# Kernel tuning notes

Measured on AMD Instinct MI355X. Metric: run time of the kernel, lower is better.

Reference implementation:

```python
import jax, jax.numpy as jnp
import numpy as np

B, S, D_MODEL, H = 2, 2048, 512, 8
DH = D_MODEL // H  # dim per head
NEG_INF = 1e9


def setup_inputs() -> dict:
    key = jax.random.key(0)
    ks = jax.random.split(key, 8)
    sc = 0.05
    return {
        "query": jax.random.normal(ks[0], (B, S, D_MODEL), jnp.float32),
        "key": jax.random.normal(ks[1], (B, S, D_MODEL), jnp.float32),
        "value": jax.random.normal(ks[2], (B, S, D_MODEL), jnp.float32),
        "mask": jnp.zeros((B, 1, S, S), jnp.float32),
        "wq": jax.random.normal(ks[3], (D_MODEL, D_MODEL), jnp.float32) * sc,
        "bq": jnp.zeros((D_MODEL,), jnp.float32),
        "wk": jax.random.normal(ks[4], (D_MODEL, D_MODEL), jnp.float32) * sc,
        "bk": jnp.zeros((D_MODEL,), jnp.float32),
        "wv": jax.random.normal(ks[5], (D_MODEL, D_MODEL), jnp.float32) * sc,
        "bv": jnp.zeros((D_MODEL,), jnp.float32),
        "wo": jax.random.normal(ks[6], (D_MODEL, D_MODEL), jnp.float32) * sc,
        "bo": jnp.zeros((D_MODEL,), jnp.float32),
    }


def _split_heads(x):
    # (B, S, D_MODEL) -> (B, H, S, DH)
    b, s, _ = x.shape
    return x.reshape(b, s, H, DH).transpose(0, 2, 1, 3)


def reference(query, key, value, mask, wq, bq, wk, bk, wv, bv, wo, bo):
    q = _split_heads(query @ wq + bq)
    k = _split_heads(key @ wk + bk)
    v = _split_heads(value @ wv + bv)
    # scaled dot-product attention; full (B, H, S, S) scores as in original
    scores = jnp.einsum("bhqd,bhkd->bhqk", q, k) / jnp.sqrt(jnp.float32(DH))
    scores = scores + mask * (-NEG_INF)
    weights = jax.nn.softmax(scores, axis=-1)  # dropout inactive (rate=0 / eval)
    attn = jnp.einsum("bhqk,bhkd->bhqd", weights, v)
    # merge heads: (B, H, S, DH) -> (B, S, D_MODEL)
    b = attn.shape[0]
    merged = attn.transpose(0, 2, 1, 3).reshape(b, -1, D_MODEL)
    return merged @ wo + bo
```

## Files before the change

### kernel.cpp

```cpp
#include <hip/hip_runtime.h>
#include <hip/hip_bf16.h>

typedef unsigned short u16;
typedef unsigned int u32;
typedef __bf16 bf16x8 __attribute__((ext_vector_type(8)));
typedef float f32x4 __attribute__((ext_vector_type(4)));
typedef u16 u16x8 __attribute__((ext_vector_type(8)));
typedef u32 u32x2 __attribute__((ext_vector_type(2)));

#define S_LEN 2048
#define DMODEL 512
#define NHEAD 8
#define DHEAD 64
#define QSCALE 0.1803368801111204f
#define MASKC 1.4426950409e9f
#define RESCALE_THR 8.0f

static __device__ __forceinline__ u16 f2bf(float f) {
    union { float f; unsigned u; } cv; cv.f = f;
    unsigned u = cv.u;
    return (u16)((u + 0x7fffu + ((u >> 16) & 1u)) >> 16);
}
static __device__ __forceinline__ u32 pk2bf(float a, float b) {
    union { __hip_bfloat162 h; u32 u; } cv;
    float2 f2; f2.x = a; f2.y = b;
    cv.h = __float22bfloat162_rn(f2);
    return cv.u;
}
static __device__ __forceinline__ bf16x8 ld8(const u16* p) {
    return *(const bf16x8*)p;
}
static __device__ __forceinline__ float fmax3(float a, float b, float c) {
    return __builtin_fmaxf(__builtin_fmaxf(a, b), c);
}

__global__ __launch_bounds__(256) void prep_kernel(
    const float* __restrict__ q, const float* __restrict__ k, const float* __restrict__ v,
    const float* __restrict__ w0, const float* __restrict__ w1,
    const float* __restrict__ w2, const float* __restrict__ w3,
    const float* __restrict__ mask,
    u16* __restrict__ Aqkv, u16* __restrict__ wtall, int* __restrict__ flags) {
    const int p = blockIdx.x;
    const int tid = threadIdx.x;
    __shared__ float t[32][33];
    __shared__ int wred[4];
    if (p < 3072) {
        const int z = p >> 10, px = p & 1023;
        const float* in = (z == 0) ? q : (z == 1) ? k : v;
        u16* o = Aqkv + (long)z * 2097152;
        long i = ((long)px * 256 + tid) * 8;
        f32x4 a = *(const f32x4*)(in + i);
        f32x4 b = *(const f32x4*)(in + i + 4);
        u16x8 r;
#pragma unroll
        for (int j = 0; j < 4; ++j) { r[j] = f2bf(a[j]); r[4 + j] = f2bf(b[j]); }
        *(u16x8*)(o + i) = r;
    } else if (p < 4096) {
        const int p2 = p - 3072;
        const int z = p2 >> 8, rem = p2 & 255, by = rem >> 4, bx = rem & 15;
        const float* in = (z == 0) ? w0 : (z == 1) ? w1 : (z == 2) ? w2 : w3;
        u16* o = wtall + (long)(((z + 1) & 3)) * 262144;
        const int tx = tid & 31, ty = tid >> 5;
#pragma unroll
        for (int i = 0; i < 4; ++i)
            t[ty + 8 * i][tx] = in[(by * 32 + ty + 8 * i) * DMODEL + bx * 32 + tx];
        __syncthreads();
#pragma unroll
        for (int i = 0; i < 4; ++i)
            o[(bx * 32 + ty + 8 * i) * DMODEL + by * 32 + tx] = f2bf(t[tx][ty + 8 * i]);
    } else {
        const int bid = p - 4096;
        const int b = bid >> 10, qt = (bid >> 5) & 31, kt = bid & 31;
        const int r = tid >> 2, cs = tid & 3;
        const float* mp = mask + ((long)(b * S_LEN + qt * 64 + r)) * S_LEN + kt * 64 + cs * 16;
        int nz = 0;
#pragma unroll
        for (int j = 0; j < 4; ++j) {
            f32x4 a = *(const f32x4*)(mp + j * 4);
            nz |= (a[0] != 0.f) | (a[1] != 0.f) | (a[2] != 0.f) | (a[3] != 0.f);
        }
        unsigned long long ball = __ballot(nz);
        if ((tid & 63) == 0) wred[tid >> 6] = (ball != 0ull) ? 1 : 0;
        __syncthreads();
        if (tid == 0) flags[bid] = wred[0] | wred[1] | wred[2] | wred[3];
    }
}

template <bool F32OUT, int TM>
static __device__ __forceinline__ void store_c(f32x4 (&acc)[TM][2],
                                               const float* __restrict__ bias,
                                               void* __restrict__ Cp, float oscale,
                                               bool vtout, int m0, int n0, int cidx, int kg) {
    if (vtout) {
        const int bb = m0 >> 11;
#pragma unroll
        for (int j = 0; j < 2; ++j) {
            int col = n0 + j * 16 + cidx;
            float bv = bias[col];
            u16* vt = (u16*)Cp + (((long)(bb * 8 + (col >> 6))) * 64 + (col & 63)) * S_LEN;
#pragma unroll
            for (int i = 0; i < TM; ++i) {
                int s = (m0 + i * 16 + kg * 4) & (S_LEN - 1);
                u32x2 d;
                d[0] = pk2bf(acc[i][j][0] + bv, acc[i][j][1] + bv);
                d[1] = pk2bf(acc[i][j][2] + bv, acc[i][j][3] + bv);
                *(u32x2*)(vt + s) = d;
            }
        }
        return;
    }
#pragma unroll
    for (int j = 0; j < 2; ++j) {
        int col = n0 + j * 16 + cidx;
        float bv = bias[col];
#pragma unroll
        for (int i = 0; i < TM; ++i) {
#pragma unroll
            for (int r = 0; r < 4; ++r) {
                int row = m0 + i * 16 + kg * 4 + r;
                float val = (acc[i][j][r] + bv) * oscale;
                if (F32OUT) {
                    ((float*)Cp)[(long)row * DMODEL + col] = val;
                } else {
                    ((u16*)Cp)[(long)row * DMODEL + col] = f2bf(val);
                }
            }
        }
    }
}

template <int BM, bool F32OUT>
static __device__ __forceinline__ void gemm_lds(const u16* __restrict__ Ag,
                                                const u16* __restrict__ Wg,
                                                const float* __restrict__ bias,
                                                void* __restrict__ Cp, float oscale,
                                                bool vtout, int bx, int by) {
    constexpr int MR = BM / 32;
    constexpr int NCH = BM / 64 + 1;
    __shared__ __align__(16) u16 As[2][BM][40];
    __shared__ __align__(16) u16 Bs[2][64][40];

    const int tid = threadIdx.x;
    const int lane = tid & 63;
    const int wave = tid >> 6;
    const int wr = wave >> 1, wc = wave & 1;
    const int cidx = lane & 15;
    const int kg = lane >> 4;

    const u16* gsrc[NCH];
    u16* ld0[NCH];
    u16* ld1[NCH];
#pragma unroll
    for (int j = 0; j < NCH; ++j) {
        int c = tid + 256 * j;
        if (c < BM * 4) {
            int r = c >> 2, s = c & 3;
            gsrc[j] = Ag + (long)(by * BM + r) * DMODEL + s * 8;
            ld0[j] = &As[0][r][s * 8];
            ld1[j] = &As[1][r][s * 8];
        } else {
            int c2 = c - BM * 4;
            int r = c2 >> 2, s = c2 & 3;
            gsrc[j] = Wg + (long)(bx * 64 + r) * DMODEL + s * 8;
            ld0[j] = &Bs[0][r][s * 8];
            ld1[j] = &Bs[1][r][s * 8];
        }
    }

    u16x8 rg[NCH];
#pragma unroll
    for (int j = 0; j < NCH; ++j) rg[j] = *(const u16x8*)(gsrc[j]);
#pragma unroll
    for (int j = 0; j < NCH; ++j) *(u16x8*)(ld0[j]) = rg[j];
#pragma unroll
    for (int j = 0; j < NCH; ++j) rg[j] = *(const u16x8*)(gsrc[j] + 32);
    __syncthreads();

    const f32x4 fz = {0.f, 0.f, 0.f, 0.f};
    f32x4 acc[MR][2];
#pragma unroll
    for (int i = 0; i < MR; ++i)
#pragma unroll
        for (int j = 0; j < 2; ++j) acc[i][j] = fz;

    const int mw = wr * (BM / 2);
    const int nw = wc * 32;

#pragma unroll 2
    for (int t = 0; t < 16; ++t) {
        const int cur = t & 1;
        if (t + 1 < 16) {
#pragma unroll
            for (int j = 0; j < NCH; ++j) *(u16x8*)((cur ? ld0 : ld1)[j]) = rg[j];
            if (t + 2 < 16) {
#pragma unroll
                for (int j = 0; j < NCH; ++j) rg[j] = *(const u16x8*)(gsrc[j] + (t + 2) * 32);
            }
        }
        bf16x8 a[MR], b[2];
#pragma unroll
        for (int i = 0; i < MR; ++i) a[i] = ld8(&As[cur][mw + i * 16 + cidx][kg * 8]);
#pragma unroll
        for (int j = 0; j < 2; ++j) b[j] = ld8(&Bs[cur][nw + j * 16 + cidx][kg * 8]);
        __builtin_amdgcn_s_setprio(1);
#pragma unroll
        for (int i = 0; i < MR; ++i)
#pragma unroll
            for (int j = 0; j < 2; ++j)
                acc[i][j] = __builtin_amdgcn_mfma_f32_16x16x32_bf16(a[i], b[j], acc[i][j], 0, 0, 0);
        __builtin_amdgcn_s_setprio(0);
        __syncthreads();
    }

    store_c<F32OUT, MR>(acc, bias, Cp, oscale, vtout, by * BM + mw, bx * 64 + nw, cidx, kg);
}

static __device__ __forceinline__ void xcd_swizzle(int gridX, int gridY, int& bx, int& by) {
    const int flat = blockIdx.x + gridX * blockIdx.y;
    const int xcd = flat & 7;
    const int j = flat >> 3;
    by = xcd * (gridY >> 3) + j / gridX;
    bx = j % gridX;
}

__global__ __launch_bounds__(256) void qkv_gemm_kernel(
    const u16* __restrict__ Aqkv,
    const u16* __restrict__ wtall,
    const float* __restrict__ bq, const float* __restrict__ bk, const float* __restrict__ bv,
    u16* __restrict__ Q, u16* __restrict__ K, u16* __restrict__ Vt) {
    const u16* A = Aqkv + (long)blockIdx.z * 2097152;
    const u16* W = wtall + (long)(blockIdx.z + 1) * 262144;
    const float* b;
    u16* C;
    float sc = 1.f;
    bool vt = false;
    if (blockIdx.z == 0) { b = bq; C = Q; sc = QSCALE; }
    else if (blockIdx.z == 1) { b = bk; C = K; }
    else { b = bv; C = Vt; vt = true; }
    int bx, by;
    xcd_swizzle(8, 32, bx, by);
    gemm_lds<128, false>(A, W, b, C, sc, vt, bx, by);
}

__global__ __launch_bounds__(256) void out_gemm_kernel(const u16* __restrict__ A,
                                                       const u16* __restrict__ Wt,
                                                       const float* __restrict__ bias,
                                                       float* __restrict__ C) {
    int bx, by;
    xcd_swizzle(8, 64, bx, by);
    gemm_lds<64, true>(A, Wt, bias, C, 1.f, false, bx, by);
}

__global__ __launch_bounds__(256) void attn_kernel(const u16* __restrict__ Q,
                                                   const u16* __restrict__ K,
                                                   const u16* __restrict__ Vt,
                                                   const float* __restrict__ mask,
                                                   const int* __restrict__ flags,
                                                   u16* __restrict__ Ab) {
    const int tid = threadIdx.x;
    const int lane = tid & 63;
    const int wave = tid >> 6;
    const int cidx = lane & 15;
    const int kg = lane >> 4;
    const int flat = blockIdx.x + 32 * blockIdx.y;
    const int F = (flat & 7) * 64 + (flat >> 3);
    const int qt = F & 31;
    const int bh = F >> 5;
    const int b = bh >> 3, h = bh & 7;
    const int q0 = qt * 64 + wave * 16;

    __shared__ u16 kt_lds[2][64 * 64];
    __shared__ u16 vt_lds[2][64 * 64];
    __shared__ u16 p_lds[4][16 * 64];
    u16* pw = p_lds[wave];

    const long qbase = ((long)(b * S_LEN + q0 + cidx)) * DMODEL + h * DHEAD + kg * 8;
    bf16x8 aq0 = ld8(Q + qbase);
    bf16x8 aq1 = ld8(Q + qbase + 32);

    bf16x8 onesf;
    {
        u16x8 t8;
        u16 ob = (cidx == 0) ? (u16)0x3F80 : (u16)0;
#pragma unroll
        for (int j = 0; j < 8; ++j) t8[j] = ob;
        onesf = *(bf16x8*)&t8;
    }

    const f32x4 fz = {0.f, 0.f, 0.f, 0.f};
    f32x4 acc[4];
#pragma unroll
    for (int nt = 0; nt < 4; ++nt) acc[nt] = fz;
    f32x4 accL = fz;
    float mrow = -1e30f;

    const int krow0 = tid >> 3, kseg0 = tid & 7;
    const int krow1 = krow0 + 32;
    const u16* kgbase = K + ((long)(b * S_LEN)) * DMODEL + h * DHEAD;
    const u16* vgbase = Vt + ((long)bh * DHEAD) * S_LEN;
    const int kd0 = krow0 * 64 + (((kseg0 ^ (krow0 & 7))) << 3);
    const int kd1 = krow1 * 64 + (((kseg0 ^ (krow1 & 7))) << 3);
    const int* flagrow = flags + b * 1024 + qt * 32;
    const int NIT = S_LEN / 64;

    const u16* kp0 = kgbase + (long)krow0 * DMODEL + kseg0 * 8;
    const u16* kp1 = kgbase + (long)krow1 * DMODEL + kseg0 * 8;
    const u16* vp0 = vgbase + (long)krow0 * S_LEN + kseg0 * 8;
    const u16* vp1 = vgbase + (long)krow1 * S_LEN + kseg0 * 8;

    u16x8 rk0 = *(const u16x8*)kp0;
    u16x8 rk1 = *(const u16x8*)kp1;
    u16x8 rv0 = *(const u16x8*)vp0;
    u16x8 rv1 = *(const u16x8*)vp1;
    *(u16x8*)&kt_lds[0][kd0] = rk0;
    *(u16x8*)&kt_lds[0][kd1] = rk1;
    *(u16x8*)&vt_lds[0][kd0] = rv0;
    *(u16x8*)&vt_lds[0][kd1] = rv1;
    rk0 = *(const u16x8*)(kp0 + 64 * DMODEL);
    rk1 = *(const u16x8*)(kp1 + 64 * DMODEL);
    rv0 = *(const u16x8*)(vp0 + 64);
    rv1 = *(const u16x8*)(vp1 + 64);
    __syncthreads();

#define ATTN_TILE(IT, CUR)                                                                 \
    {                                                                                      \
        if ((IT) + 1 < NIT) {                                                              \
            u16* kn = kt_lds[(CUR) ^ 1];                                                   \
            u16* vn = vt_lds[(CUR) ^ 1];                                                   \
            *(u16x8*)&kn[kd0] = rk0;                                                       \
            *(u16x8*)&kn[kd1] = rk1;                                                       \
            *(u16x8*)&vn[kd0] = rv0;                                                       \
            *(u16x8*)&vn[kd1] = rv1;                                                       \
            if ((IT) + 2 < NIT) {                                                          \
                const int t2 = ((IT) + 2) * 64;                                            \
                rk0 = *(const u16x8*)(kp0 + (long)t2 * DMODEL);                            \
                rk1 = *(const u16x8*)(kp1 + (long)t2 * DMODEL);                            \
                rv0 = *(const u16x8*)(vp0 + t2);                                           \
                rv1 = *(const u16x8*)(vp1 + t2);                                           \
            }                                                                              \
        }                                                                                  \
        const int flg = flagrow[(IT)];                                                     \
        const u16* kb = kt_lds[(CUR)];                                                     \
        const u16* vb = vt_lds[(CUR)];                                                     \
        f32x4 sacc[4];                                                                     \
        _Pragma("unroll")                                                                  \
        for (int ct = 0; ct < 4; ++ct) sacc[ct] = fz;                                      \
        __builtin_amdgcn_s_setprio(1);                                                     \
        _Pragma("unroll")                                                                  \
        for (int ct = 0; ct < 4; ++ct) {                                                   \
            int r = ct * 16 + cidx;                                                        \
            bf16x8 kv0 = ld8(&kb[r * 64 + ((kg ^ (r & 7)) << 3)]);                         \
            bf16x8 kv1 = ld8(&kb[r * 64 + (((4 ^ kg) ^ (r & 7)) << 3)]);                   \
            sacc[ct] = __builtin_amdgcn_mfma_f32_16x16x32_bf16(kv0, aq0, sacc[ct], 0, 0, 0); \
            sacc[ct] = __builtin_amdgcn_mfma_f32_16x16x32_bf16(kv1, aq1, sacc[ct], 0, 0, 0); \
        }                                                                                  \
        __builtin_amdgcn_s_setprio(0);                                                     \
        if (flg) {                                                                         \
            const float* mb = mask + ((long)(b * S_LEN + q0 + cidx)) * S_LEN + (IT) * 64 + kg * 4; \
            _Pragma("unroll")                                                              \
            for (int ct = 0; ct < 4; ++ct) {                                               \
                f32x4 mv = *(const f32x4*)(mb + ct * 16);                                  \
                _Pragma("unroll")                                                          \
                for (int r = 0; r < 4; ++r) sacc[ct][r] -= MASKC * mv[r];                  \
            }                                                                              \
        }                                                                                  \
        float t0 = fmax3(sacc[0][0], sacc[0][1], sacc[0][2]);                              \
        float t1 = fmax3(sacc[0][3], sacc[1][0], sacc[1][1]);                              \
        float t2 = fmax3(sacc[1][2], sacc[1][3], sacc[2][0]);                              \
        float t3 = fmax3(sacc[2][1], sacc[2][2], sacc[2][3]);                              \
        float t4 = fmax3(sacc[3][0], sacc[3][1], sacc[3][2]);                              \
        float mxl = __builtin_fmaxf(fmax3(fmax3(t0, t1, t2), t3, t4), sacc[3][3]);         \
        if (__any(mxl > mrow + RESCALE_THR)) {                                             \
            float mx = fmaxf(mxl, __shfl_xor(mxl, 16));                                    \
            mx = fmaxf(mx, __shfl_xor(mx, 32));                                            \
            float mnew = fmaxf(mrow, mx);                                                  \
            float alpha = __builtin_amdgcn_exp2f(mrow - mnew);                             \
            mrow = mnew;                                                                   \
            accL = accL * alpha;                                                           \
            _Pragma("unroll")                                                              \
            for (int nt = 0; nt < 4; ++nt) acc[nt] = acc[nt] * alpha;                      \
        }                                                                                  \
        _Pragma("unroll")                                                                  \
        for (int ct = 0; ct < 4; ++ct)                                                     \
            _Pragma("unroll")                                                              \
            for (int r = 0; r < 4; ++r)                                                    \
                sacc[ct][r] = __builtin_amdgcn_exp2f(sacc[ct][r] - mrow);                  \
        _Pragma("unroll")                                                                  \
        for (int ct = 0; ct < 4; ++ct) {                                                   \
            u32x2 d;                                                                       \
            d[0] = pk2bf(sacc[ct][0], sacc[ct][1]);                                        \
            d[1] = pk2bf(sacc[ct][2], sacc[ct][3]);                                        \
            int blk = 2 * ct + (kg >> 1);                                                  \
            *(u32x2*)&pw[cidx * 64 + ((blk ^ (cidx & 7)) << 3) + (kg & 1) * 4] = d;        \
        }                                                                                  \
        bf16x8 pf0 = ld8(&pw[cidx * 64 + ((kg ^ (cidx & 7)) << 3)]);                       \
        bf16x8 pf1 = ld8(&pw[cidx * 64 + (((4 ^ kg) ^ (cidx & 7)) << 3)]);                 \
        __builtin_amdgcn_s_setprio(1);                                                     \
        _Pragma("unroll")                                                                  \
        for (int nt = 0; nt < 4; ++nt) {                                                   \
            int rr = nt * 16 + cidx;                                                       \
            bf16x8 v0 = ld8(&vb[rr * 64 + ((kg ^ (rr & 7)) << 3)]);                        \
            bf16x8 v1 = ld8(&vb[rr * 64 + (((4 ^ kg) ^ (rr & 7)) << 3)]);                  \
            acc[nt] = __builtin_amdgcn_mfma_f32_16x16x32_bf16(v0, pf0, acc[nt], 0, 0, 0);  \
            acc[nt] = __builtin_amdgcn_mfma_f32_16x16x32_bf16(v1, pf1, acc[nt], 0, 0, 0);  \
        }                                                                                  \
        accL = __builtin_amdgcn_mfma_f32_16x16x32_bf16(onesf, pf0, accL, 0, 0, 0);         \
        accL = __builtin_amdgcn_mfma_f32_16x16x32_bf16(onesf, pf1, accL, 0, 0, 0);         \
        __builtin_amdgcn_s_setprio(0);                                                     \
        __syncthreads();                                                                   \
    }

    for (int it = 0; it < NIT; it += 2) {
        ATTN_TILE(it, 0)
        ATTN_TILE(it + 1, 1)
    }
#undef ATTN_TILE

    float Lb = __shfl(accL[0], cidx);
    float invL = 1.f / Lb;
    const long abase = ((long)(b * S_LEN + q0 + cidx)) * DMODEL + h * DHEAD;
#pragma unroll
    for (int nt = 0; nt < 4; ++nt) {
        u32x2 d;
        d[0] = pk2bf(acc[nt][0] * invL, acc[nt][1] * invL);
        d[1] = pk2bf(acc[nt][2] * invL, acc[nt][3] * invL);
        *(u32x2*)(Ab + abase + nt * 16 + kg * 4) = d;
    }
}

extern "C" void kernel_launch(void* const* d_in, const int* in_sizes, int n_in,
                              void* d_out, int out_size, void* d_ws, size_t ws_size,
                              hipStream_t stream) {
    const float* q_in = (const float*)d_in[0];
    const float* k_in = (const float*)d_in[1];
    const float* v_in = (const float*)d_in[2];
    const float* mask = (const float*)d_in[3];
    const float* wq = (const float*)d_in[4];
    const float* bq = (const float*)d_in[5];
    const float* wk = (const float*)d_in[6];
    const float* bk = (const float*)d_in[7];
    const float* wv = (const float*)d_in[8];
    const float* bv = (const float*)d_in[9];
    const float* wo = (const float*)d_in[10];
    const float* bo = (const float*)d_in[11];

    u16* ws = (u16*)d_ws;
    u16* Qb = ws;
    u16* Kb = Qb + 2097152;
    u16* Vt = Kb + 2097152;
    u16* wtall = Vt + 2097152;
    u16* Sreg = wtall + 4 * 262144;
    u16* Ab = Sreg + 3 * 2097152;
    int* mflags = (int*)(Ab + 2097152);

    prep_kernel<<<6144, 256, 0, stream>>>(q_in, k_in, v_in, wq, wk, wv, wo, mask,
                                          Sreg, wtall, mflags);
    qkv_gemm_kernel<<<dim3(8, 32, 3), 256, 0, stream>>>(Sreg, wtall, bq, bk, bv, Qb, Kb, Vt);
    attn_kernel<<<dim3(32, 16), 256, 0, stream>>>(Qb, Kb, Vt, mask, mflags, Ab);
    out_gemm_kernel<<<dim3(8, 64), 256, 0, stream>>>(Ab, wtall, bo, (float*)d_out);
}
```

Before: 171.2 us.

## Fuse fp32-to-bf16 activation conversion into QKV GEMM loads; shrink out-GEMM tile

The QKV projection GEMM now reads the fp32 query/key/value inputs directly and converts them to bf16 in registers before writing to LDS. This removes the separate conversion pass in the prep kernel and the intermediate bf16 buffer, saving a full read/write round trip of the three activations. The output GEMM moves to a 32-row tile with twice as many blocks, so the generic GEMM loader gains validity masks for partial chunks. The fused kernel loads twice as many bytes per A element from global memory and spends extra VALU work converting inside the main loop.

```diff
diff --git a/kernel.cpp b/kernel.cpp
--- a/kernel.cpp
+++ b/kernel.cpp
@@ -7,6 +7,7 @@
 typedef float f32x4 __attribute__((ext_vector_type(4)));
 typedef u16 u16x8 __attribute__((ext_vector_type(8)));
 typedef u32 u32x2 __attribute__((ext_vector_type(2)));
+typedef u32 u32x4 __attribute__((ext_vector_type(4)));
 
 #define S_LEN 2048
 #define DMODEL 512
@@ -30,34 +31,27 @@
 static __device__ __forceinline__ bf16x8 ld8(const u16* p) {
     return *(const bf16x8*)p;
 }
+static __device__ __forceinline__ u16x8 cvt8(f32x4 a, f32x4 b) {
+    union { u32x4 u; u16x8 s; } cv;
+    cv.u[0] = pk2bf(a[0], a[1]); cv.u[1] = pk2bf(a[2], a[3]);
+    cv.u[2] = pk2bf(b[0], b[1]); cv.u[3] = pk2bf(b[2], b[3]);
+    return cv.s;
+}
 static __device__ __forceinline__ float fmax3(float a, float b, float c) {
     return __builtin_fmaxf(__builtin_fmaxf(a, b), c);
 }
 
 __global__ __launch_bounds__(256) void prep_kernel(
-    const float* __restrict__ q, const float* __restrict__ k, const float* __restrict__ v,
     const float* __restrict__ w0, const float* __restrict__ w1,
     const float* __restrict__ w2, const float* __restrict__ w3,
     const float* __restrict__ mask,
-    u16* __restrict__ Aqkv, u16* __restrict__ wtall, int* __restrict__ flags) {
+    u16* __restrict__ wtall, int* __restrict__ flags) {
     const int p = blockIdx.x;
     const int tid = threadIdx.x;
     __shared__ float t[32][33];
     __shared__ int wred[4];
-    if (p < 3072) {
-        const int z = p >> 10, px = p & 1023;
-        const float* in = (z == 0) ? q : (z == 1) ? k : v;
-        u16* o = Aqkv + (long)z * 2097152;
-        long i = ((long)px * 256 + tid) * 8;
-        f32x4 a = *(const f32x4*)(in + i);
-        f32x4 b = *(const f32x4*)(in + i + 4);
-        u16x8 r;
-#pragma unroll
-        for (int j = 0; j < 4; ++j) { r[j] = f2bf(a[j]); r[4 + j] = f2bf(b[j]); }
-        *(u16x8*)(o + i) = r;
-    } else if (p < 4096) {
-        const int p2 = p - 3072;
-        const int z = p2 >> 8, rem = p2 & 255, by = rem >> 4, bx = rem & 15;
+    if (p < 1024) {
+        const int z = p >> 8, rem = p & 255, by = rem >> 4, bx = rem & 15;
         const float* in = (z == 0) ? w0 : (z == 1) ? w1 : (z == 2) ? w2 : w3;
         u16* o = wtall + (long)(((z + 1) & 3)) * 262144;
         const int tx = tid & 31, ty = tid >> 5;
@@ -69,7 +63,7 @@
         for (int i = 0; i < 4; ++i)
             o[(bx * 32 + ty + 8 * i) * DMODEL + by * 32 + tx] = f2bf(t[tx][ty + 8 * i]);
     } else {
-        const int bid = p - 4096;
+        const int bid = p - 1024;
         const int b = bid >> 10, qt = (bid >> 5) & 31, kt = bid & 31;
         const int r = tid >> 2, cs = tid & 3;
         const float* mp = mask + ((long)(b * S_LEN + qt * 64 + r)) * S_LEN + kt * 64 + cs * 16;
@@ -129,6 +123,14 @@
     }
 }
 
+static __device__ __forceinline__ void xcd_swizzle(int gridX, int gridY, int& bx, int& by) {
+    const int flat = blockIdx.x + gridX * blockIdx.y;
+    const int xcd = flat & 7;
+    const int j = flat >> 3;
+    by = xcd * (gridY >> 3) + j / gridX;
+    bx = j % gridX;
+}
+
 template <int BM, bool F32OUT>
 static __device__ __forceinline__ void gemm_lds(const u16* __restrict__ Ag,
                                                 const u16* __restrict__ Wg,
@@ -136,7 +138,8 @@
                                                 void* __restrict__ Cp, float oscale,
                                                 bool vtout, int bx, int by) {
     constexpr int MR = BM / 32;
-    constexpr int NCH = BM / 64 + 1;
+    constexpr int TOT = BM * 4 + 256;
+    constexpr int NCH = (TOT + 255) / 256;
     __shared__ __align__(16) u16 As[2][BM][40];
     __shared__ __align__(16) u16 Bs[2][64][40];
 
@@ -150,16 +153,19 @@
     const u16* gsrc[NCH];
     u16* ld0[NCH];
     u16* ld1[NCH];
+    bool val[NCH];
 #pragma unroll
     for (int j = 0; j < NCH; ++j) {
         int c = tid + 256 * j;
-        if (c < BM * 4) {
-            int r = c >> 2, s = c & 3;
+        val[j] = (c < TOT);
+        int cc = val[j] ? c : 0;
+        if (cc < BM * 4) {
+            int r = cc >> 2, s = cc & 3;
             gsrc[j] = Ag + (long)(by * BM + r) * DMODEL + s * 8;
             ld0[j] = &As[0][r][s * 8];
             ld1[j] = &As[1][r][s * 8];
         } else {
-            int c2 = c - BM * 4;
+            int c2 = cc - BM * 4;
             int r = c2 >> 2, s = c2 & 3;
             gsrc[j] = Wg + (long)(bx * 64 + r) * DMODEL + s * 8;
             ld0[j] = &Bs[0][r][s * 8];
@@ -169,11 +175,11 @@
 
     u16x8 rg[NCH];
 #pragma unroll
-    for (int j = 0; j < NCH; ++j) rg[j] = *(const u16x8*)(gsrc[j]);
-#pragma unroll
-    for (int j = 0; j < NCH; ++j) *(u16x8*)(ld0[j]) = rg[j];
-#pragma unroll
-    for (int j = 0; j < NCH; ++j) rg[j] = *(const u16x8*)(gsrc[j] + 32);
+    for (int j = 0; j < NCH; ++j) if (val[j]) rg[j] = *(const u16x8*)(gsrc[j]);
+#pragma unroll
+    for (int j = 0; j < NCH; ++j) if (val[j]) *(u16x8*)(ld0[j]) = rg[j];
+#pragma unroll
+    for (int j = 0; j < NCH; ++j) if (val[j]) rg[j] = *(const u16x8*)(gsrc[j] + 32);
     __syncthreads();
 
     const f32x4 fz = {0.f, 0.f, 0.f, 0.f};
@@ -191,10 +197,11 @@
         const int cur = t & 1;
         if (t + 1 < 16) {
 #pragma unroll
-            for (int j = 0; j < NCH; ++j) *(u16x8*)((cur ? ld0 : ld1)[j]) = rg[j];
+            for (int j = 0; j < NCH; ++j) if (val[j]) *(u16x8*)((cur ? ld0 : ld1)[j]) = rg[j];
             if (t + 2 < 16) {
 #pragma unroll
-                for (int j = 0; j < NCH; ++j) rg[j] = *(const u16x8*)(gsrc[j] + (t + 2) * 32);
+                for (int j = 0; j < NCH; ++j)
+                    if (val[j]) rg[j] = *(const u16x8*)(gsrc[j] + (t + 2) * 32);
             }
         }
         bf16x8 a[MR], b[2];
@@ -215,31 +222,93 @@
     store_c<F32OUT, MR>(acc, bias, Cp, oscale, vtout, by * BM + mw, bx * 64 + nw, cidx, kg);
 }
 
-static __device__ __forceinline__ void xcd_swizzle(int gridX, int gridY, int& bx, int& by) {
-    const int flat = blockIdx.x + gridX * blockIdx.y;
-    const int xcd = flat & 7;
-    const int j = flat >> 3;
-    by = xcd * (gridY >> 3) + j / gridX;
-    bx = j % gridX;
-}
-
 __global__ __launch_bounds__(256) void qkv_gemm_kernel(
-    const u16* __restrict__ Aqkv,
+    const float* __restrict__ Aq, const float* __restrict__ Ak, const float* __restrict__ Av,
     const u16* __restrict__ wtall,
     const float* __restrict__ bq, const float* __restrict__ bk, const float* __restrict__ bv,
     u16* __restrict__ Q, u16* __restrict__ K, u16* __restrict__ Vt) {
-    const u16* A = Aqkv + (long)blockIdx.z * 2097152;
-    const u16* W = wtall + (long)(blockIdx.z + 1) * 262144;
-    const float* b;
-    u16* C;
+    const float* A = (blockIdx.z == 0) ? Aq : (blockIdx.z == 1) ? Ak : Av;
+    const u16* Wg = wtall + (long)(blockIdx.z + 1) * 262144;
+    const float* bias;
+    u16* Cp;
     float sc = 1.f;
     bool vt = false;
-    if (blockIdx.z == 0) { b = bq; C = Q; sc = QSCALE; }
-    else if (blockIdx.z == 1) { b = bk; C = K; }
-    else { b = bv; C = Vt; vt = true; }
+    if (blockIdx.z == 0) { bias = bq; Cp = Q; sc = QSCALE; }
+    else if (blockIdx.z == 1) { bias = bk; Cp = K; }
+    else { bias = bv; Cp = Vt; vt = true; }
     int bx, by;
     xcd_swizzle(8, 32, bx, by);
-    gemm_lds<128, false>(A, W, b, C, sc, vt, bx, by);
+
+    __shared__ __align__(16) u16 As[2][128][40];
+    __shared__ __align__(16) u16 Bs[2][64][40];
+
+    const int tid = threadIdx.x;
+    const int lane = tid & 63;
+    const int wave = tid >> 6;
+    const int wr = wave >> 1, wc = wave & 1;
+    const int cidx = lane & 15;
+    const int kg = lane >> 4;
+    const int r0 = tid >> 2, s0 = tid & 3;
+
+    const float* ga0 = A + (long)(by * 128 + r0) * DMODEL + s0 * 8;
+    const float* ga1 = ga0 + (long)64 * DMODEL;
+    const u16* gb = Wg + (long)(bx * 64 + r0) * DMODEL + s0 * 8;
+    u16* wa0[2] = {&As[0][r0][s0 * 8], &As[1][r0][s0 * 8]};
+    u16* wa1[2] = {&As[0][64 + r0][s0 * 8], &As[1][64 + r0][s0 * 8]};
+    u16* wb[2] = {&Bs[0][r0][s0 * 8], &Bs[1][r0][s0 * 8]};
+
+    f32x4 ra0a = *(const f32x4*)ga0, ra0b = *(const f32x4*)(ga0 + 4);
+    f32x4 ra1a = *(const f32x4*)ga1, ra1b = *(const f32x4*)(ga1 + 4);
+    u16x8 rb = *(const u16x8*)gb;
+    *(u16x8*)wa0[0] = cvt8(ra0a, ra0b);
+    *(u16x8*)wa1[0] = cvt8(ra1a, ra1b);
+    *(u16x8*)wb[0] = rb;
+    ra0a = *(const f32x4*)(ga0 + 32); ra0b = *(const f32x4*)(ga0 + 36);
+    ra1a = *(const f32x4*)(ga1 + 32); ra1b = *(const f32x4*)(ga1 + 36);
+    rb = *(const u16x8*)(gb + 32);
+    __syncthreads();
+
+    const f32x4 fz = {0.f, 0.f, 0.f, 0.f};
+    f32x4 acc[4][2];
+#pragma unroll
+    for (int i = 0; i < 4; ++i)
+#pragma unroll
+        for (int j = 0; j < 2; ++j) acc[i][j] = fz;
+
+    const int mw = wr * 64;
+    const int nw = wc * 32;
+
+#pragma unroll 2
+    for (int t = 0; t < 16; ++t) {
+        const int cur = t & 1;
+        if (t + 1 < 16) {
+            const int nb = cur ^ 1;
+            *(u16x8*)wa0[nb] = cvt8(ra0a, ra0b);
+            *(u16x8*)wa1[nb] = cvt8(ra1a, ra1b);
+            *(u16x8*)wb[nb] = rb;
+            if (t + 2 < 16) {
+                const int o = (t + 2) * 32;
+                ra0a = *(const f32x4*)(ga0 + o); ra0b = *(const f32x4*)(ga0 + o + 4);
+                ra1a = *(const f32x4*)(ga1 + o); ra1b = *(const f32x4*)(ga1 + o + 4);
+                rb = *(const u16x8*)(gb + o);
+            }
+        }
+        bf16x8 a[4], b[2];
+#pragma unroll
+        for (int i = 0; i < 4; ++i) a[i] = ld8(&As[cur][mw + i * 16 + cidx][kg * 8]);
+#pragma unroll
+        for (int j = 0; j < 2; ++j) b[j] = ld8(&Bs[cur][nw + j * 16 + cidx][kg * 8]);
+        __builtin_amdgcn_s_setprio(1);
+#pragma unroll
+        for (int i = 0; i < 4; ++i)
+#pragma unroll
+            for (int j = 0; j < 2; ++j)
+                acc[i][j] = __builtin_amdgcn_mfma_f32_16x16x32_bf16(a[i], b[j], acc[i][j], 0, 0, 0);
+        __builtin_amdgcn_s_setprio(0);
+        __syncthreads();
+    }
+
+    store_c<false, 4>(acc, bias, Cp, sc, vt, by * 128 + mw, bx * 64 + nw, cidx, kg);
 }
 
 __global__ __launch_bounds__(256) void out_gemm_kernel(const u16* __restrict__ A,
@@ -247,8 +316,8 @@
                                                        const float* __restrict__ bias,
                                                        float* __restrict__ C) {
     int bx, by;
-    xcd_swizzle(8, 64, bx, by);
-    gemm_lds<64, true>(A, Wt, bias, C, 1.f, false, bx, by);
+    xcd_swizzle(8, 128, bx, by);
+    gemm_lds<32, true>(A, Wt, bias, C, 1.f, false, bx, by);
 }
 
 __global__ __launch_bounds__(256) void attn_kernel(const u16* __restrict__ Q,
@@ -449,13 +518,12 @@
     u16* Kb = Qb + 2097152;
     u16* Vt = Kb + 2097152;
     u16* wtall = Vt + 2097152;
-    u16* Sreg = wtall + 4 * 262144;
-    u16* Ab = Sreg + 3 * 2097152;
+    u16* Ab = wtall + 4 * 262144;
     int* mflags = (int*)(Ab + 2097152);
 
-    prep_kernel<<<6144, 256, 0, stream>>>(q_in, k_in, v_in, wq, wk, wv, wo, mask,
-                                          Sreg, wtall, mflags);
-    qkv_gemm_kernel<<<dim3(8, 32, 3), 256, 0, stream>>>(Sreg, wtall, bq, bk, bv, Qb, Kb, Vt);
+    prep_kernel<<<3072, 256, 0, stream>>>(wq, wk, wv, wo, mask, wtall, mflags);
+    qkv_gemm_kernel<<<dim3(8, 32, 3), 256, 0, stream>>>(q_in, k_in, v_in, wtall,
+                                                        bq, bk, bv, Qb, Kb, Vt);
     attn_kernel<<<dim3(32, 16), 256, 0, stream>>>(Qb, Kb, Vt, mask, mflags, Ab);
-    out_gemm_kernel<<<dim3(8, 64), 256, 0, stream>>>(Ab, wtall, bo, (float*)d_out);
-}
+    out_gemm_kernel<<<dim3(8, 128), 256, 0, stream>>>(Ab, wtall, bo, (float*)d_out);
+}
```

New measurement: 174.0 us. About the same (+1.6%).

## Use direct global-to-LDS loads for GEMM and attention tile staging

Applied to the files above, without the earlier changes.

Replaces register-staged global loads followed by LDS stores with global_load_lds 16-byte transfers in both the projection GEMM and the attention K/V tile loads. To match the linear LDS destination of these loads, the XOR swizzle moves from the LDS address to the global source address. The GEMM LDS padding is dropped in favour of this swizzle. The goal is to cut VGPR pressure and the extra ds_write instructions. The risk is that the prefetch distance shrinks to one tile, and the synchronisation relies on __syncthreads waiting for the async LDS loads.

```diff
diff --git a/kernel.cpp b/kernel.cpp
--- a/kernel.cpp
+++ b/kernel.cpp
@@ -32,6 +32,11 @@
 }
 static __device__ __forceinline__ float fmax3(float a, float b, float c) {
     return __builtin_fmaxf(__builtin_fmaxf(a, b), c);
+}
+static __device__ __forceinline__ void gll16(const void* g, void* l) {
+    __builtin_amdgcn_global_load_lds(
+        (const __attribute__((address_space(1))) void*)g,
+        (__attribute__((address_space(3))) void*)l, 16, 0, 0);
 }
 
 __global__ __launch_bounds__(256) void prep_kernel(
@@ -136,9 +141,12 @@
                                                 void* __restrict__ Cp, float oscale,
                                                 bool vtout, int bx, int by) {
     constexpr int MR = BM / 32;
-    constexpr int NCH = BM / 64 + 1;
-    __shared__ __align__(16) u16 As[2][BM][40];
-    __shared__ __align__(16) u16 Bs[2][64][40];
+    constexpr int ACH = BM * 4;
+    constexpr int TOT = ACH + 256;
+    constexpr int NCH = TOT / 256;
+    static_assert(TOT % 256 == 0, "chunk count must tile 256 threads");
+    __shared__ __align__(16) u16 As[2][BM][32];
+    __shared__ __align__(16) u16 Bs[2][64][32];
 
     const int tid = threadIdx.x;
     const int lane = tid & 63;
@@ -148,32 +156,28 @@
     const int kg = lane >> 4;
 
     const u16* gsrc[NCH];
-    u16* ld0[NCH];
-    u16* ld1[NCH];
+    u16* ldst[NCH][2];
 #pragma unroll
     for (int j = 0; j < NCH; ++j) {
         int c = tid + 256 * j;
-        if (c < BM * 4) {
+        if (c < ACH) {
             int r = c >> 2, s = c & 3;
-            gsrc[j] = Ag + (long)(by * BM + r) * DMODEL + s * 8;
-            ld0[j] = &As[0][r][s * 8];
-            ld1[j] = &As[1][r][s * 8];
+            int sg = s ^ ((r >> 1) & 3);
+            gsrc[j] = Ag + (long)(by * BM + r) * DMODEL + sg * 8;
+            ldst[j][0] = &As[0][0][0] + c * 8;
+            ldst[j][1] = &As[1][0][0] + c * 8;
         } else {
-            int c2 = c - BM * 4;
+            int c2 = c - ACH;
             int r = c2 >> 2, s = c2 & 3;
-            gsrc[j] = Wg + (long)(bx * 64 + r) * DMODEL + s * 8;
-            ld0[j] = &Bs[0][r][s * 8];
-            ld1[j] = &Bs[1][r][s * 8];
-        }
-    }
-
-    u16x8 rg[NCH];
-#pragma unroll
-    for (int j = 0; j < NCH; ++j) rg[j] = *(const u16x8*)(gsrc[j]);
-#pragma unroll
-    for (int j = 0; j < NCH; ++j) *(u16x8*)(ld0[j]) = rg[j];
-#pragma unroll
-    for (int j = 0; j < NCH; ++j) rg[j] = *(const u16x8*)(gsrc[j] + 32);
+            int sg = s ^ ((r >> 1) & 3);
+            gsrc[j] = Wg + (long)(bx * 64 + r) * DMODEL + sg * 8;
+            ldst[j][0] = &Bs[0][0][0] + c2 * 8;
+            ldst[j][1] = &Bs[1][0][0] + c2 * 8;
+        }
+    }
+
+#pragma unroll
+    for (int j = 0; j < NCH; ++j) gll16(gsrc[j], ldst[j][0]);
     __syncthreads();
 
     const f32x4 fz = {0.f, 0.f, 0.f, 0.f};
@@ -191,17 +195,19 @@
         const int cur = t & 1;
         if (t + 1 < 16) {
 #pragma unroll
-            for (int j = 0; j < NCH; ++j) *(u16x8*)((cur ? ld0 : ld1)[j]) = rg[j];
-            if (t + 2 < 16) {
-#pragma unroll
-                for (int j = 0; j < NCH; ++j) rg[j] = *(const u16x8*)(gsrc[j] + (t + 2) * 32);
-            }
+            for (int j = 0; j < NCH; ++j) gll16(gsrc[j] + (t + 1) * 32, ldst[j][cur ^ 1]);
         }
         bf16x8 a[MR], b[2];
 #pragma unroll
-        for (int i = 0; i < MR; ++i) a[i] = ld8(&As[cur][mw + i * 16 + cidx][kg * 8]);
-#pragma unroll
-        for (int j = 0; j < 2; ++j) b[j] = ld8(&Bs[cur][nw + j * 16 + cidx][kg * 8]);
+        for (int i = 0; i < MR; ++i) {
+            int rl = mw + i * 16 + cidx;
+            a[i] = ld8(&As[cur][rl][(kg ^ ((rl >> 1) & 3)) * 8]);
+        }
+#pragma unroll
+        for (int j = 0; j < 2; ++j) {
+            int rl = nw + j * 16 + cidx;
+            b[j] = ld8(&Bs[cur][rl][(kg ^ ((rl >> 1) & 3)) * 8]);
+        }
         __builtin_amdgcn_s_setprio(1);
 #pragma unroll
         for (int i = 0; i < MR; ++i)
@@ -269,8 +275,8 @@
     const int b = bh >> 3, h = bh & 7;
     const int q0 = qt * 64 + wave * 16;
 
-    __shared__ u16 kt_lds[2][64 * 64];
-    __shared__ u16 vt_lds[2][64 * 64];
+    __shared__ __align__(16) u16 kt_lds[2][64 * 64];
+    __shared__ __align__(16) u16 vt_lds[2][64 * 64];
     __shared__ u16 p_lds[4][16 * 64];
     u16* pw = p_lds[wave];
 
@@ -298,46 +304,32 @@
     const int krow1 = krow0 + 32;
     const u16* kgbase = K + ((long)(b * S_LEN)) * DMODEL + h * DHEAD;
     const u16* vgbase = Vt + ((long)bh * DHEAD) * S_LEN;
-    const int kd0 = krow0 * 64 + (((kseg0 ^ (krow0 & 7))) << 3);
-    const int kd1 = krow1 * 64 + (((kseg0 ^ (krow1 & 7))) << 3);
+    const int sg0 = kseg0 ^ (krow0 & 7);
+    const int sg1 = kseg0 ^ (krow1 & 7);
     const int* flagrow = flags + b * 1024 + qt * 32;
     const int NIT = S_LEN / 64;
 
-    const u16* kp0 = kgbase + (long)krow0 * DMODEL + kseg0 * 8;
-    const u16* kp1 = kgbase + (long)krow1 * DMODEL + kseg0 * 8;
-    const u16* vp0 = vgbase + (long)krow0 * S_LEN + kseg0 * 8;
-    const u16* vp1 = vgbase + (long)krow1 * S_LEN + kseg0 * 8;
-
-    u16x8 rk0 = *(const u16x8*)kp0;
-    u16x8 rk1 = *(const u16x8*)kp1;
-    u16x8 rv0 = *(const u16x8*)vp0;
-    u16x8 rv1 = *(const u16x8*)vp1;
-    *(u16x8*)&kt_lds[0][kd0] = rk0;
-    *(u16x8*)&kt_lds[0][kd1] = rk1;
-    *(u16x8*)&vt_lds[0][kd0] = rv0;
-    *(u16x8*)&vt_lds[0][kd1] = rv1;
-    rk0 = *(const u16x8*)(kp0 + 64 * DMODEL);
-    rk1 = *(const u16x8*)(kp1 + 64 * DMODEL);
-    rv0 = *(const u16x8*)(vp0 + 64);
-    rv1 = *(const u16x8*)(vp1 + 64);
+    const u16* kp0 = kgbase + (long)krow0 * DMODEL + sg0 * 8;
+    const u16* kp1 = kgbase + (long)krow1 * DMODEL + sg1 * 8;
+    const u16* vp0 = vgbase + (long)krow0 * S_LEN + sg0 * 8;
+    const u16* vp1 = vgbase + (long)krow1 * S_LEN + sg1 * 8;
+
+    gll16(kp0, &kt_lds[0][tid * 8]);
+    gll16(kp1, &kt_lds[0][2048 + tid * 8]);
+    gll16(vp0, &vt_lds[0][tid * 8]);
+    gll16(vp1, &vt_lds[0][2048 + tid * 8]);
     __syncthreads();
 
 #define ATTN_TILE(IT, CUR)                                                                 \
     {                                                                                      \
         if ((IT) + 1 < NIT) {                                                              \
+            const int tn = ((IT) + 1) * 64;                                                \
             u16* kn = kt_lds[(CUR) ^ 1];                                                   \
             u16* vn = vt_lds[(CUR) ^ 1];                                                   \
-            *(u16x8*)&kn[kd0] = rk0;                                                       \
-            *(u16x8*)&kn[kd1] = rk1;                                                       \
-            *(u16x8*)&vn[kd0] = rv0;                                                       \
-            *(u16x8*)&vn[kd1] = rv1;                                                       \
-            if ((IT) + 2 < NIT) {                                                          \
-                const int t2 = ((IT) + 2) * 64;                                            \
-                rk0 = *(const u16x8*)(kp0 + (long)t2 * DMODEL);                            \
-                rk1 = *(const u16x8*)(kp1 + (long)t2 * DMODEL);                            \
-                rv0 = *(const u16x8*)(vp0 + t2);                                           \
-                rv1 = *(const u16x8*)(vp1 + t2);                                           \
-            }                                                                              \
+            gll16(kp0 + (long)tn * DMODEL, &kn[tid * 8]);                                  \
+            gll16(kp1 + (long)tn * DMODEL, &kn[2048 + tid * 8]);                           \
+            gll16(vp0 + tn, &vn[tid * 8]);                                                 \
+            gll16(vp1 + tn, &vn[2048 + tid * 8]);                                          \
         }                                                                                  \
         const int flg = flagrow[(IT)];                                                     \
         const u16* kb = kt_lds[(CUR)];                                                     \
@@ -407,7 +399,7 @@
         accL = __builtin_amdgcn_mfma_f32_16x16x32_bf16(onesf, pf0, accL, 0, 0, 0);         \
         accL = __builtin_amdgcn_mfma_f32_16x16x32_bf16(onesf, pf1, accL, 0, 0, 0);         \
         __builtin_amdgcn_s_setprio(0);                                                     \
-        __syncthreads();                                                                   \
+        __syncthreads();                \
     }
 
     for (int it = 0; it < NIT; it += 2) {
```

Result: no change. 173.0 us (+1.1%).
